# Performance work log

Measured on AMD Instinct MI355X. Metric: run time of the kernel, lower is better.

## Reference

```python
import jax, jax.numpy as jnp
import numpy as np

B, C, H, W = 2, 320, 48, 48
HEADS, DIM_HEAD, NUM_FILTERS = 8, 64, 32
INNER = HEADS * DIM_HEAD  # 512
LN_EPS = 1e-05


def setup_inputs() -> dict:
    key = jax.random.key(0)
    ks = jax.random.split(key, 8)
    w = 0.02
    return {
        "hidden_states": jax.random.normal(ks[0], (B, C, H, W), jnp.float32),
        "encoder_hidden_states": jax.random.normal(ks[1], (B, C, H, W), jnp.float32),
        "Wq": jax.random.normal(ks[2], (C, INNER), jnp.float32) * w,
        "Wk": jax.random.normal(ks[3], (C, INNER), jnp.float32) * w,
        "Wv": jax.random.normal(ks[4], (C, INNER), jnp.float32) * w,
        "Wo": jax.random.normal(ks[5], (INNER, C), jnp.float32) * w,
        "bo": jnp.zeros((C,), jnp.float32),
        "ln_gamma": jnp.ones((C,), jnp.float32),
        "ln_beta": jnp.zeros((C,), jnp.float32),
        "ex_filters": jax.random.normal(ks[6], (NUM_FILTERS, INNER), jnp.float32),
        "dist_filters": jax.random.normal(ks[7], (NUM_FILTERS, INNER), jnp.float32),
        "scale": jnp.ones((1,), jnp.float32),  # learnable scale shadows dim_head**-0.5
    }


def _split_heads(t, heads):
    b, s, d = t.shape
    return t.reshape(b, s, heads, d // heads).transpose(0, 2, 1, 3)  # [b,h,s,dh]


def reference(hidden_states, encoder_hidden_states, Wq, Wk, Wv, Wo, bo,
              ln_gamma, ln_beta, ex_filters, dist_filters, scale):
    b, c, h, w = hidden_states.shape
    _, _, rh, rw = encoder_hidden_states.shape
    residual = hidden_states
    s = scale[0]

    hs = hidden_states.transpose(0, 2, 3, 1).reshape(b, h * w, c)        # [b, q, C]
    ehs = encoder_hidden_states.transpose(0, 2, 3, 1).reshape(b, rh * rw, c)

    # LayerNorm on encoder states
    mu = ehs.mean(-1, keepdims=True)
    var = jnp.mean((ehs - mu) ** 2, axis=-1, keepdims=True)
    ehs = (ehs - mu) * jax.lax.rsqrt(var + LN_EPS) * ln_gamma + ln_beta

    q = _split_heads(hs @ Wq, HEADS)    # [b,h,q,dh]
    k = _split_heads(ehs @ Wk, HEADS)   # [b,h,kv,dh]
    v = _split_heads(ehs @ Wv, HEADS)   # [b,h,kv,dh]
    ef = _split_heads(jnp.broadcast_to(ex_filters[None], (b,) + ex_filters.shape), HEADS)   # [b,h,F,dh]
    df = _split_heads(jnp.broadcast_to(dist_filters[None], (b,) + dist_filters.shape), HEADS)

    # spatial attention: softmax over kv positions
    spatial = jax.nn.softmax(jnp.einsum('bhfd,bhkd->bhfk', ef, k) * s, axis=-1)   # [b,h,F,kv]
    # channel attention: softmax over the filter axis (torch dim=1 of [B*h, F, q])
    channel = jax.nn.softmax(jnp.einsum('bhfd,bhqd->bhfq', df, q) * s, axis=2)    # [b,h,F,q]

    attn = jnp.einsum('bhfq,bhfk->bhqk', channel, spatial)                        # [b,h,q,kv]
    out = jnp.einsum('bhqk,bhkd->bhqd', attn, v)                                  # [b,h,q,dh]

    out = out.transpose(0, 2, 1, 3).reshape(b, h * w, INNER)
    out = out @ Wo + bo
    out = out.reshape(b, h, w, c).transpose(0, 3, 1, 2)
    return out + residual * s
```

## Files before the change

### kernel.cpp

```cpp
#include <hip/hip_runtime.h>
#include <math.h>

#define Bc 2
#define Cc 320
#define Pc 2304
#define HEADSc 8
#define DHc 64
#define INNERc 512
#define Fc 32
#define LN_EPS 1e-5f
#define CHUNKS 18
#define CHUNK_P (Pc / CHUNKS)

typedef __attribute__((ext_vector_type(8))) short bf16x8;
typedef __attribute__((ext_vector_type(4))) float f32x4;

static __device__ __forceinline__ ushort f2bf(float x) {
  uint u = __builtin_bit_cast(uint, x);
  u = (u + 0x7fffu + ((u >> 16) & 1u)) >> 16;
  return (ushort)u;
}
static __device__ __forceinline__ float bf2f(ushort u) {
  return __builtin_bit_cast(float, ((uint)u) << 16);
}

__global__ __launch_bounds__(256) void stats_kernel(
    const float* __restrict__ ehs, float* __restrict__ mu,
    float* __restrict__ rstd) {
  int lane = threadIdx.x & 63, g = threadIdx.x >> 6;
  int gp = blockIdx.x * 64 + lane;
  int b = gp / Pc, p = gp % Pc;
  const float* base = ehs + (size_t)b * Cc * Pc + p;
  float sum = 0.f, sumsq = 0.f;
  for (int c = g * 80; c < (g + 1) * 80; ++c) {
    float x = base[(size_t)c * Pc];
    sum += x; sumsq += x * x;
  }
  __shared__ float s1[4][64], s2[4][64];
  s1[g][lane] = sum; s2[g][lane] = sumsq;
  __syncthreads();
  if (threadIdx.x < 64) {
    int l = threadIdx.x;
    float ts = s1[0][l] + s1[1][l] + s1[2][l] + s1[3][l];
    float tq = s2[0][l] + s2[1][l] + s2[2][l] + s2[3][l];
    float mean = ts / (float)Cc;
    float var = tq / (float)Cc - mean * mean;
    int gp2 = blockIdx.x * 64 + l;
    mu[gp2] = mean;
    rstd[gp2] = rsqrtf(var + LN_EPS);
  }
}

static __device__ void transpose_tile(const float* __restrict__ src,
                                      ushort* __restrict__ dst, int R, int C,
                                      int r0, int c0, int tid,
                                      float (*t)[65]) {
#pragma unroll
  for (int it = 0; it < 4; ++it) {
    int lin = it * 256 + tid;
    int rr = lin >> 4, c4 = lin & 15;
    float4 v = *(const float4*)(&src[(size_t)(r0 + rr) * C + c0 + c4 * 4]);
    t[rr][c4 * 4 + 0] = v.x; t[rr][c4 * 4 + 1] = v.y;
    t[rr][c4 * 4 + 2] = v.z; t[rr][c4 * 4 + 3] = v.w;
  }
  __syncthreads();
#pragma unroll
  for (int it = 0; it < 2; ++it) {
    int lin = it * 256 + tid;
    int cc = lin >> 3, r8 = lin & 7;
    ushort tmp[8];
#pragma unroll
    for (int j = 0; j < 8; ++j) tmp[j] = f2bf(t[r8 * 8 + j][cc]);
    *(uint4*)(&dst[(size_t)(c0 + cc) * R + r0 + r8 * 8]) = *(const uint4*)tmp;
  }
}

__global__ __launch_bounds__(256) void transpose_act_kernel(
    const float* __restrict__ hs, const float* __restrict__ ehs,
    const float* __restrict__ mu, const float* __restrict__ rstd,
    const float* __restrict__ gamma, const float* __restrict__ beta,
    ushort* __restrict__ hsT, ushort* __restrict__ ehsT) {
  __shared__ float t[64][65];
  __shared__ float lmu[64], lrs[64], lgam[64], lbet[64];
  int z = blockIdx.z, b = z & 1, which = z >> 1;
  int r0 = blockIdx.y * 64, c0 = blockIdx.x * 64;
  int tid = threadIdx.x;
  const float* src = (which ? ehs : hs) + (size_t)b * Cc * Pc;
  ushort* dst = (which ? ehsT : hsT) + (size_t)b * Pc * Cc;
  if (which && tid < 64) {
    lmu[tid] = mu[b * Pc + c0 + tid];
    lrs[tid] = rstd[b * Pc + c0 + tid];
    lgam[tid] = gamma[r0 + tid];
    lbet[tid] = beta[r0 + tid];
  }
#pragma unroll
  for (int it = 0; it < 4; ++it) {
    int lin = it * 256 + tid;
    int rr = lin >> 4, c4 = lin & 15;
    float4 v = *(const float4*)(&src[(size_t)(r0 + rr) * Pc + c0 + c4 * 4]);
    t[rr][c4 * 4 + 0] = v.x; t[rr][c4 * 4 + 1] = v.y;
    t[rr][c4 * 4 + 2] = v.z; t[rr][c4 * 4 + 3] = v.w;
  }
  __syncthreads();
#pragma unroll
  for (int it = 0; it < 2; ++it) {
    int lin = it * 256 + tid;
    int cc = lin >> 3, r8 = lin & 7;
    ushort tmp[8];
    float m_ = which ? lmu[cc] : 0.f, rs_ = which ? lrs[cc] : 1.f;
#pragma unroll
    for (int j = 0; j < 8; ++j) {
      int ch = r8 * 8 + j;
      float x = t[ch][cc];
      float val = which ? (x - m_) * rs_ * lgam[ch] + lbet[ch] : x;
      tmp[j] = f2bf(val);
    }
    *(uint4*)(&dst[(size_t)(c0 + cc) * Cc + r0 + r8 * 8]) = *(const uint4*)tmp;
  }
}

__global__ __launch_bounds__(256) void prep_w_kernel(
    const float* __restrict__ Wv, const float* __restrict__ Wo,
    const float* __restrict__ exf, const float* __restrict__ Wk,
    const float* __restrict__ dif, const float* __restrict__ Wq,
    ushort* __restrict__ WvT, ushort* __restrict__ WoT,
    ushort* __restrict__ Gk, ushort* __restrict__ Gq) {
  __shared__ float smem[32 * 66 + 64 * 65];
  int idx = blockIdx.x, tid = threadIdx.x;
  if (idx < 40) {
    float (*t)[65] = (float(*)[65])smem;
    transpose_tile(Wv, WvT, Cc, INNERc, (idx / 8) * 64, (idx % 8) * 64, tid, t);
  } else if (idx < 80) {
    int i = idx - 40;
    float (*t)[65] = (float(*)[65])smem;
    transpose_tile(Wo, WoT, INNERc, Cc, (i / 5) * 64, (i % 5) * 64, tid, t);
  } else {
    int i = idx - 80;
    int c0 = (i % 5) * 64, h = (i / 5) % 8, zz = i / 40;
    const float* filt = zz ? dif : exf;
    const float* W = zz ? Wq : Wk;
    ushort* G = zz ? Gq : Gk;
    float (*ef)[66] = (float(*)[66])smem;
    float (*wk)[65] = (float(*)[65])(smem + 32 * 66);
    for (int l = tid; l < Fc * DHc; l += 256) {
      int f = l >> 6, d = l & 63;
      ef[f][d] = filt[(size_t)f * INNERc + h * 64 + d];
    }
    for (int l = tid; l < 64 * DHc; l += 256) {
      int cc = l >> 6, d = l & 63;
      wk[cc][d] = W[(size_t)(c0 + cc) * INNERc + h * 64 + d];
    }
    __syncthreads();
    int f = tid >> 3, cbase = tid & 7;
    float acc[8] = {};
#pragma unroll
    for (int d4 = 0; d4 < DHc; d4 += 4) {
      float4 a = *(const float4*)(&ef[f][d4]);
#pragma unroll
      for (int j = 0; j < 8; ++j) {
        float4 b = *(const float4*)(&wk[cbase + j * 8][d4]);
        acc[j] += a.x * b.x + a.y * b.y + a.z * b.z + a.w * b.w;
      }
    }
#pragma unroll
    for (int j = 0; j < 8; ++j)
      G[(size_t)(h * Fc + f) * Cc + c0 + cbase + j * 8] = f2bf(acc[j]);
  }
}

__global__ __launch_bounds__(256) void gemm_all_kernel(
    const ushort* __restrict__ WvT, const ushort* __restrict__ Gk,
    const ushort* __restrict__ Gq, const ushort* __restrict__ ehsT,
    const ushort* __restrict__ hsT, ushort* __restrict__ Vt,
    float* __restrict__ L1, float* __restrict__ Lc) {
  const int K = Cc;
  int b = blockIdx.z, y = blockIdx.y;
  const ushort* A;
  const ushort* Bt;
  ushort* OutB = nullptr;
  float* OutF = nullptr;
  if (y < 8) {
    int m0 = y * 64;
    A = WvT + (size_t)m0 * K; Bt = ehsT;
    OutB = Vt + ((size_t)b * INNERc + m0) * Pc;
  } else if (y < 12) {
    int m0 = (y - 8) * 64;
    A = Gk + (size_t)m0 * K; Bt = ehsT;
    OutF = L1 + ((size_t)b * 256 + m0) * Pc;
  } else {
    int m0 = (y - 12) * 64;
    A = Gq + (size_t)m0 * K; Bt = hsT;
    OutF = Lc + ((size_t)b * 256 + m0) * Pc;
  }
  int n0 = blockIdx.x * 128;
  int tid = threadIdx.x, lane = tid & 63, wv = tid >> 6;
  int l15 = lane & 15, kq = lane >> 4;
  __shared__ alignas(16) ushort As[64 * 64];
  __shared__ alignas(16) ushort Bs[128 * 64];
  const ushort* Bb = Bt + ((size_t)b * Pc + n0) * K;

  f32x4 acc[4][2] = {};
  for (int k0 = 0; k0 < K; k0 += 64) {
#pragma unroll
    for (int it = 0; it < 2; ++it) {
      int lin = it * 256 + tid;
      int row = lin >> 3, p = lin & 7;
      int lc = p ^ (row & 7);
      *(uint4*)(&As[row * 64 + p * 8]) =
          *(const uint4*)(A + (size_t)row * K + k0 + lc * 8);
    }
#pragma unroll
    for (int it = 0; it < 4; ++it) {
      int lin = it * 256 + tid;
      int row = lin >> 3, p = lin & 7;
      int lc = p ^ (row & 7);
      *(uint4*)(&Bs[row * 64 + p * 8]) =
          *(const uint4*)(Bb + (size_t)row * K + k0 + lc * 8);
    }
    __syncthreads();
#pragma unroll
    for (int s = 0; s < 2; ++s) {
      bf16x8 af[4], bfr[2];
#pragma unroll
      for (int mt = 0; mt < 4; ++mt) {
        int m = mt * 16 + l15;
        int p = (s * 4 + kq) ^ (m & 7);
        af[mt] = *(const bf16x8*)(&As[m * 64 + p * 8]);
      }
#pragma unroll
      for (int nt = 0; nt < 2; ++nt) {
        int n = wv * 32 + nt * 16 + l15;
        int p = (s * 4 + kq) ^ (n & 7);
        bfr[nt] = *(const bf16x8*)(&Bs[n * 64 + p * 8]);
      }
#pragma unroll
      for (int mt = 0; mt < 4; ++mt)
#pragma unroll
        for (int nt = 0; nt < 2; ++nt)
          acc[mt][nt] = __builtin_amdgcn_mfma_f32_16x16x32_bf16(
              af[mt], bfr[nt], acc[mt][nt], 0, 0, 0);
    }
    __syncthreads();
  }
  if (OutB) {
#pragma unroll
    for (int mt = 0; mt < 4; ++mt)
#pragma unroll
      for (int nt = 0; nt < 2; ++nt) {
        int ncol = n0 + wv * 32 + nt * 16 + l15;
#pragma unroll
        for (int r = 0; r < 4; ++r) {
          int m = mt * 16 + kq * 4 + r;
          OutB[(size_t)m * Pc + ncol] = f2bf(acc[mt][nt][r]);
        }
      }
  } else {
#pragma unroll
    for (int mt = 0; mt < 4; ++mt)
#pragma unroll
      for (int nt = 0; nt < 2; ++nt) {
        int ncol = n0 + wv * 32 + nt * 16 + l15;
#pragma unroll
        for (int r = 0; r < 4; ++r) {
          int m = mt * 16 + kq * 4 + r;
          OutF[(size_t)m * Pc + ncol] = acc[mt][nt][r];
        }
      }
  }
}

__global__ __launch_bounds__(256) void rowstat_kernel(
    const float* __restrict__ L, const float* __restrict__ scale_p,
    float* __restrict__ rowm, float* __restrict__ rowinv) {
  __shared__ float red[4];
  float s = scale_p[0];
  const float* Lr = L + (size_t)blockIdx.x * Pc;
  int tid = threadIdx.x, lane = tid & 63, wv = tid >> 6;
  float vals[9];
  float m = -1e30f;
#pragma unroll
  for (int i = 0; i < 9; ++i) {
    vals[i] = Lr[tid + 256 * i] * s;
    m = fmaxf(m, vals[i]);
  }
#pragma unroll
  for (int o = 32; o > 0; o >>= 1) m = fmaxf(m, __shfl_xor(m, o));
  if (lane == 0) red[wv] = m;
  __syncthreads();
  m = fmaxf(fmaxf(red[0], red[1]), fmaxf(red[2], red[3]));
  __syncthreads();
  float sum = 0.f;
#pragma unroll
  for (int i = 0; i < 9; ++i) sum += __expf(vals[i] - m);
#pragma unroll
  for (int o = 32; o > 0; o >>= 1) sum += __shfl_xor(sum, o);
  if (lane == 0) red[wv] = sum;
  __syncthreads();
  if (tid == 0) {
    sum = red[0] + red[1] + red[2] + red[3];
    rowm[blockIdx.x] = m;
    rowinv[blockIdx.x] = 1.f / sum;
  }
}

__global__ __launch_bounds__(256) void sv_part_kernel(
    const float* __restrict__ L1, const ushort* __restrict__ Vt,
    const float* __restrict__ rowm, const float* __restrict__ rowinv,
    const float* __restrict__ scale_p, float* __restrict__ svp) {
  int b = blockIdx.z, h = blockIdx.y, c = blockIdx.x;
  int tid = threadIdx.x;
  int tx = tid & 15, ty = tid >> 4;
  int p0base = c * CHUNK_P;
  const float* sp = L1 + ((size_t)(b * HEADSc + h)) * Fc * Pc;
  const ushort* vb = Vt + ((size_t)b * INNERc + h * DHc) * Pc;

  __shared__ float sp_s[64][34];
  __shared__ float v_s[64][68];
  __shared__ float lm[Fc], li[Fc];
  if (tid < Fc) {
    int row0 = (b * HEADSc + h) * Fc;
    lm[tid] = rowm[row0 + tid];
    li[tid] = rowinv[row0 + tid];
  }
  __syncthreads();
  float s = scale_p[0];

  float acc[2][4] = {};
  for (int t = 0; t < CHUNK_P; t += 64) {
    int p0 = p0base + t;
    for (int l = tid; l < Fc * 64; l += 256) {
      int f = l >> 6, pp = l & 63;
      float raw = sp[(size_t)f * Pc + p0 + pp];
      sp_s[pp][f] = __expf(s * raw - lm[f]) * li[f];
    }
    for (int l = tid; l < DHc * 64; l += 256) {
      int d = l >> 6, pp = l & 63;
      v_s[pp][d] = bf2f(vb[(size_t)d * Pc + p0 + pp]);
    }
    __syncthreads();
#pragma unroll
    for (int kk = 0; kk < 64; ++kk) {
      float2 a = *reinterpret_cast<const float2*>(&sp_s[kk][ty * 2]);
      float4 bv = *reinterpret_cast<const float4*>(&v_s[kk][tx * 4]);
      acc[0][0] += a.x * bv.x; acc[0][1] += a.x * bv.y;
      acc[0][2] += a.x * bv.z; acc[0][3] += a.x * bv.w;
      acc[1][0] += a.y * bv.x; acc[1][1] += a.y * bv.y;
      acc[1][2] += a.y * bv.z; acc[1][3] += a.y * bv.w;
    }
    __syncthreads();
  }
  int bh = b * HEADSc + h;
  float* op = svp + ((size_t)c * 16 + bh) * (Fc * DHc);
#pragma unroll
  for (int i = 0; i < 2; ++i) {
    int f = ty * 2 + i;
    *reinterpret_cast<float4*>(&op[(size_t)f * DHc + tx * 4]) =
        make_float4(acc[i][0], acc[i][1], acc[i][2], acc[i][3]);
  }
}

__global__ __launch_bounds__(256) void sv_reduce_kernel(
    const float* __restrict__ svp, float* __restrict__ sv) {
  int idx = blockIdx.x * 256 + threadIdx.x;
  float s = 0.f;
#pragma unroll
  for (int c = 0; c < CHUNKS; ++c) s += svp[(size_t)c * 32768 + idx];
  sv[idx] = s;
}

__global__ __launch_bounds__(256) void oa_kernel(
    const float* __restrict__ Lc, const float* __restrict__ sv,
    const float* __restrict__ scale_p, ushort* __restrict__ OAT) {
  int b = blockIdx.z, h = blockIdx.y;
  int tid = threadIdx.x;
  int lane = tid & 63, wv = tid >> 6;
  int pos0 = blockIdx.x * 64;
  float s = scale_p[0];
  __shared__ float svl[Fc][DHc];
  __shared__ float tile[64][65];
  for (int l = tid; l < Fc * DHc; l += 256)
    svl[l >> 6][l & 63] = sv[((size_t)(b * HEADSc + h)) * Fc * DHc + l];
  __syncthreads();
  const float* ch = Lc + (((size_t)(b * HEADSc + h)) * Fc) * Pc + pos0 + lane;
  float v[Fc];
  float m = -1e30f;
#pragma unroll
  for (int f = 0; f < Fc; ++f) {
    v[f] = ch[(size_t)f * Pc] * s;
    m = fmaxf(m, v[f]);
  }
  float sum = 0.f;
#pragma unroll
  for (int f = 0; f < Fc; ++f) {
    v[f] = __expf(v[f] - m);
    sum += v[f];
  }
  float inv = 1.f / sum;
  float acc[16] = {};
#pragma unroll
  for (int f = 0; f < Fc; ++f) {
    float cf = v[f] * inv;
#pragma unroll
    for (int dd = 0; dd < 16; ++dd) acc[dd] += cf * svl[f][wv * 16 + dd];
  }
#pragma unroll
  for (int dd = 0; dd < 16; ++dd) tile[lane][wv * 16 + dd] = acc[dd];
  __syncthreads();
#pragma unroll
  for (int it = 0; it < 2; ++it) {
    int lin = it * 256 + tid;
    int p = lin >> 3, c8 = lin & 7;
    ushort tmp[8];
#pragma unroll
    for (int j = 0; j < 8; ++j) tmp[j] = f2bf(tile[p][c8 * 8 + j]);
    *(uint4*)(&OAT[((size_t)b * Pc + pos0 + p) * INNERc + h * DHc + c8 * 8]) =
        *(const uint4*)tmp;
  }
}

__global__ __launch_bounds__(256) void gemm_mfma_kernel(
    const ushort* __restrict__ A, const ushort* __restrict__ Bt,
    float* __restrict__ Out, int K, int Mdim,
    const float* __restrict__ bias, const float* __restrict__ res,
    const float* __restrict__ scale_p) {
  int b = blockIdx.z;
  int n0 = blockIdx.x * 128, m0 = blockIdx.y * 64;
  int tid = threadIdx.x, lane = tid & 63, wv = tid >> 6;
  int l15 = lane & 15, kq = lane >> 4;
  __shared__ alignas(16) ushort As[64 * 64];
  __shared__ alignas(16) ushort Bs[128 * 64];
  const ushort* Ab = A + (size_t)m0 * K;
  const ushort* Bb = Bt + ((size_t)b * Pc + n0) * K;

  f32x4 acc[4][2] = {};
  for (int k0 = 0; k0 < K; k0 += 64) {
#pragma unroll
    for (int it = 0; it < 2; ++it) {
      int lin = it * 256 + tid;
      int row = lin >> 3, p = lin & 7;
      int lc = p ^ (row & 7);
      *(uint4*)(&As[row * 64 + p * 8]) =
          *(const uint4*)(Ab + (size_t)row * K + k0 + lc * 8);
    }
#pragma unroll
    for (int it = 0; it < 4; ++it) {
      int lin = it * 256 + tid;
      int row = lin >> 3, p = lin & 7;
      int lc = p ^ (row & 7);
      *(uint4*)(&Bs[row * 64 + p * 8]) =
          *(const uint4*)(Bb + (size_t)row * K + k0 + lc * 8);
    }
    __syncthreads();
#pragma unroll
    for (int s = 0; s < 2; ++s) {
      bf16x8 af[4], bfr[2];
#pragma unroll
      for (int mt = 0; mt < 4; ++mt) {
        int m = mt * 16 + l15;
        int p = (s * 4 + kq) ^ (m & 7);
        af[mt] = *(const bf16x8*)(&As[m * 64 + p * 8]);
      }
#pragma unroll
      for (int nt = 0; nt < 2; ++nt) {
        int n = wv * 32 + nt * 16 + l15;
        int p = (s * 4 + kq) ^ (n & 7);
        bfr[nt] = *(const bf16x8*)(&Bs[n * 64 + p * 8]);
      }
#pragma unroll
      for (int mt = 0; mt < 4; ++mt)
#pragma unroll
        for (int nt = 0; nt < 2; ++nt)
          acc[mt][nt] = __builtin_amdgcn_mfma_f32_16x16x32_bf16(
              af[mt], bfr[nt], acc[mt][nt], 0, 0, 0);
    }
    __syncthreads();
  }
  float s = scale_p[0];
  float* Ob = Out + ((size_t)b * Mdim + m0) * Pc + n0;
  const float* rb = res + ((size_t)b * Mdim + m0) * Pc + n0;
#pragma unroll
  for (int mt = 0; mt < 4; ++mt)
#pragma unroll
    for (int nt = 0; nt < 2; ++nt) {
      int ncol = wv * 32 + nt * 16 + l15;
#pragma unroll
      for (int r = 0; r < 4; ++r) {
        int m = mt * 16 + kq * 4 + r;
        Ob[(size_t)m * Pc + ncol] =
            acc[mt][nt][r] + bias[m0 + m] + s * rb[(size_t)m * Pc + ncol];
      }
    }
}

extern "C" void kernel_launch(void* const* d_in, const int* in_sizes, int n_in,
                              void* d_out, int out_size, void* d_ws, size_t ws_size,
                              hipStream_t stream) {
  const float* hs    = (const float*)d_in[0];
  const float* ehs   = (const float*)d_in[1];
  const float* Wq    = (const float*)d_in[2];
  const float* Wk    = (const float*)d_in[3];
  const float* Wv    = (const float*)d_in[4];
  const float* Wo    = (const float*)d_in[5];
  const float* bo    = (const float*)d_in[6];
  const float* gamma = (const float*)d_in[7];
  const float* beta  = (const float*)d_in[8];
  const float* exf   = (const float*)d_in[9];
  const float* dif   = (const float*)d_in[10];
  const float* scale = (const float*)d_in[11];
  float* out = (float*)d_out;

  float* ws = (float*)d_ws;
  float* L1   = ws;
  float* Lc   = L1 + 1179648;
  float* sv   = Lc + 1179648;
  float* svp  = sv + 32768;
  float* mu   = svp + 589824;
  float* rstd = mu + 4608;
  float* rowm = rstd + 4608;
  float* rowinv = rowm + 512;
  ushort* hsT  = (ushort*)(rowinv + 512);
  ushort* ehsT = hsT + 1474560;
  ushort* WvT  = ehsT + 1474560;
  ushort* WoT  = WvT + 163840;
  ushort* Gk   = WoT + 163840;
  ushort* Gq   = Gk + 81920;
  ushort* Vt   = Gq + 81920;
  ushort* OAT  = Vt + 2359296;

  stats_kernel<<<dim3((Bc * Pc) / 64), dim3(256), 0, stream>>>(ehs, mu, rstd);
  transpose_act_kernel<<<dim3(Pc / 64, Cc / 64, 4), dim3(256), 0, stream>>>(
      hs, ehs, mu, rstd, gamma, beta, hsT, ehsT);
  prep_w_kernel<<<dim3(160), dim3(256), 0, stream>>>(
      Wv, Wo, exf, Wk, dif, Wq, WvT, WoT, Gk, Gq);
  gemm_all_kernel<<<dim3(Pc / 128, 16, Bc), dim3(256), 0, stream>>>(
      WvT, Gk, Gq, ehsT, hsT, Vt, L1, Lc);
  rowstat_kernel<<<dim3(Bc * HEADSc * Fc), dim3(256), 0, stream>>>(
      L1, scale, rowm, rowinv);
  sv_part_kernel<<<dim3(CHUNKS, HEADSc, Bc), dim3(256), 0, stream>>>(
      L1, Vt, rowm, rowinv, scale, svp);
  sv_reduce_kernel<<<dim3((16 * Fc * DHc) / 256), dim3(256), 0, stream>>>(svp, sv);
  oa_kernel<<<dim3(Pc / 64, HEADSc, Bc), dim3(256), 0, stream>>>(
      Lc, sv, scale, OAT);
  gemm_mfma_kernel<<<dim3(Pc / 128, Cc / 64, Bc), dim3(256), 0, stream>>>(
      WoT, OAT, out, INNERc, Cc, bo, hs, scale);
}
```

Before: 157.3 us.

## Fuse spatial and channel softmax into GEMM kernels with online-softmax chunk merge

Splits the combined GEMM so only V is materialized. The spatial logits are computed per 128-position chunk and fed straight into a local softmax and an MFMA-based P·V product, with per-chunk max and sum merged in the reduce step. Channel logits, their softmax over filters and the multiply with the spatial-value matrix are fused into one kernel, also on MFMA. This removes the fp32 L1/Lc round trips through global memory and the separate row-statistics and scalar-FMA kernels. In exchange the probabilities are held in bf16 and the fused kernels use more shared memory and synchronisation.

```diff
diff --git a/kernel.cpp b/kernel.cpp
--- a/kernel.cpp
+++ b/kernel.cpp
@@ -10,7 +10,7 @@
 #define Fc 32
 #define LN_EPS 1e-5f
 #define CHUNKS 18
-#define CHUNK_P (Pc / CHUNKS)
+#define CHUNK_P 128
 
 typedef __attribute__((ext_vector_type(8))) short bf16x8;
 typedef __attribute__((ext_vector_type(4))) float f32x4;
@@ -19,9 +19,6 @@
   uint u = __builtin_bit_cast(uint, x);
   u = (u + 0x7fffu + ((u >> 16) & 1u)) >> 16;
   return (ushort)u;
-}
-static __device__ __forceinline__ float bf2f(ushort u) {
-  return __builtin_bit_cast(float, ((uint)u) << 16);
 }
 
 __global__ __launch_bounds__(256) void stats_kernel(
@@ -168,36 +165,17 @@
   }
 }
 
-__global__ __launch_bounds__(256) void gemm_all_kernel(
-    const ushort* __restrict__ WvT, const ushort* __restrict__ Gk,
-    const ushort* __restrict__ Gq, const ushort* __restrict__ ehsT,
-    const ushort* __restrict__ hsT, ushort* __restrict__ Vt,
-    float* __restrict__ L1, float* __restrict__ Lc) {
+__global__ __launch_bounds__(256) void gemm_v_kernel(
+    const ushort* __restrict__ WvT, const ushort* __restrict__ ehsT,
+    ushort* __restrict__ Vt) {
   const int K = Cc;
-  int b = blockIdx.z, y = blockIdx.y;
-  const ushort* A;
-  const ushort* Bt;
-  ushort* OutB = nullptr;
-  float* OutF = nullptr;
-  if (y < 8) {
-    int m0 = y * 64;
-    A = WvT + (size_t)m0 * K; Bt = ehsT;
-    OutB = Vt + ((size_t)b * INNERc + m0) * Pc;
-  } else if (y < 12) {
-    int m0 = (y - 8) * 64;
-    A = Gk + (size_t)m0 * K; Bt = ehsT;
-    OutF = L1 + ((size_t)b * 256 + m0) * Pc;
-  } else {
-    int m0 = (y - 12) * 64;
-    A = Gq + (size_t)m0 * K; Bt = hsT;
-    OutF = Lc + ((size_t)b * 256 + m0) * Pc;
-  }
-  int n0 = blockIdx.x * 128;
+  int b = blockIdx.z, m0 = blockIdx.y * 64, n0 = blockIdx.x * 128;
   int tid = threadIdx.x, lane = tid & 63, wv = tid >> 6;
   int l15 = lane & 15, kq = lane >> 4;
   __shared__ alignas(16) ushort As[64 * 64];
   __shared__ alignas(16) ushort Bs[128 * 64];
-  const ushort* Bb = Bt + ((size_t)b * Pc + n0) * K;
+  const ushort* Ab = WvT + (size_t)m0 * K;
+  const ushort* Bb = ehsT + ((size_t)b * Pc + n0) * K;
 
   f32x4 acc[4][2] = {};
   for (int k0 = 0; k0 < K; k0 += 64) {
@@ -207,7 +185,7 @@
       int row = lin >> 3, p = lin & 7;
       int lc = p ^ (row & 7);
       *(uint4*)(&As[row * 64 + p * 8]) =
-          *(const uint4*)(A + (size_t)row * K + k0 + lc * 8);
+          *(const uint4*)(Ab + (size_t)row * K + k0 + lc * 8);
     }
 #pragma unroll
     for (int it = 0; it < 4; ++it) {
@@ -219,18 +197,18 @@
     }
     __syncthreads();
 #pragma unroll
-    for (int s = 0; s < 2; ++s) {
+    for (int ss = 0; ss < 2; ++ss) {
       bf16x8 af[4], bfr[2];
 #pragma unroll
       for (int mt = 0; mt < 4; ++mt) {
         int m = mt * 16 + l15;
-        int p = (s * 4 + kq) ^ (m & 7);
+        int p = (ss * 4 + kq) ^ (m & 7);
         af[mt] = *(const bf16x8*)(&As[m * 64 + p * 8]);
       }
 #pragma unroll
       for (int nt = 0; nt < 2; ++nt) {
         int n = wv * 32 + nt * 16 + l15;
-        int p = (s * 4 + kq) ^ (n & 7);
+        int p = (ss * 4 + kq) ^ (n & 7);
         bfr[nt] = *(const bf16x8*)(&Bs[n * 64 + p * 8]);
       }
 #pragma unroll
@@ -242,179 +220,300 @@
     }
     __syncthreads();
   }
-  if (OutB) {
-#pragma unroll
-    for (int mt = 0; mt < 4; ++mt)
+  ushort* Ob = Vt + ((size_t)b * INNERc + m0) * Pc + n0;
+#pragma unroll
+  for (int mt = 0; mt < 4; ++mt)
+#pragma unroll
+    for (int nt = 0; nt < 2; ++nt) {
+      int ncol = wv * 32 + nt * 16 + l15;
+#pragma unroll
+      for (int r = 0; r < 4; ++r) {
+        int m = mt * 16 + kq * 4 + r;
+        Ob[(size_t)m * Pc + ncol] = f2bf(acc[mt][nt][r]);
+      }
+    }
+}
+
+__global__ __launch_bounds__(256) void spatial_kernel(
+    const ushort* __restrict__ Gk, const ushort* __restrict__ ehsT,
+    const ushort* __restrict__ Vt, const float* __restrict__ scale_p,
+    float* __restrict__ svp, float* __restrict__ mj, float* __restrict__ lj) {
+  int c = blockIdx.x, h = blockIdx.y, b = blockIdx.z;
+  int tid = threadIdx.x, lane = tid & 63, wv = tid >> 6;
+  int l15 = lane & 15, kq = lane >> 4;
+  int pos0 = c * CHUNK_P;
+  int bh = b * HEADSc + h;
+  float s = scale_p[0];
+
+  __shared__ alignas(16) ushort As[32 * 64];
+  __shared__ alignas(16) ushort Bs[128 * 64];
+  __shared__ float Sq[32 * 132];
+  __shared__ alignas(16) ushort P[32 * 136];
+  __shared__ alignas(16) ushort Vs[64 * 136];
+
+  const ushort* Ab = Gk + (size_t)(h * Fc) * Cc;
+  const ushort* Bb = ehsT + ((size_t)b * Pc + pos0) * Cc;
+  f32x4 acc[2][2] = {};
+  for (int k0 = 0; k0 < Cc; k0 += 64) {
+    {
+      int row = tid >> 3, p = tid & 7;
+      int lc = p ^ (row & 7);
+      *(uint4*)(&As[row * 64 + p * 8]) =
+          *(const uint4*)(Ab + (size_t)row * Cc + k0 + lc * 8);
+    }
+#pragma unroll
+    for (int it = 0; it < 4; ++it) {
+      int lin = it * 256 + tid;
+      int row = lin >> 3, p = lin & 7;
+      int lc = p ^ (row & 7);
+      *(uint4*)(&Bs[row * 64 + p * 8]) =
+          *(const uint4*)(Bb + (size_t)row * Cc + k0 + lc * 8);
+    }
+    __syncthreads();
+#pragma unroll
+    for (int ss = 0; ss < 2; ++ss) {
+      bf16x8 af[2], bfr[2];
+#pragma unroll
+      for (int mt = 0; mt < 2; ++mt) {
+        int m = mt * 16 + l15;
+        int p = (ss * 4 + kq) ^ (m & 7);
+        af[mt] = *(const bf16x8*)(&As[m * 64 + p * 8]);
+      }
 #pragma unroll
       for (int nt = 0; nt < 2; ++nt) {
-        int ncol = n0 + wv * 32 + nt * 16 + l15;
-#pragma unroll
-        for (int r = 0; r < 4; ++r) {
-          int m = mt * 16 + kq * 4 + r;
-          OutB[(size_t)m * Pc + ncol] = f2bf(acc[mt][nt][r]);
+        int n = wv * 32 + nt * 16 + l15;
+        int p = (ss * 4 + kq) ^ (n & 7);
+        bfr[nt] = *(const bf16x8*)(&Bs[n * 64 + p * 8]);
+      }
+#pragma unroll
+      for (int mt = 0; mt < 2; ++mt)
+#pragma unroll
+        for (int nt = 0; nt < 2; ++nt)
+          acc[mt][nt] = __builtin_amdgcn_mfma_f32_16x16x32_bf16(
+              af[mt], bfr[nt], acc[mt][nt], 0, 0, 0);
+    }
+    __syncthreads();
+  }
+#pragma unroll
+  for (int mt = 0; mt < 2; ++mt)
+#pragma unroll
+    for (int nt = 0; nt < 2; ++nt)
+#pragma unroll
+      for (int r = 0; r < 4; ++r)
+        Sq[(mt * 16 + kq * 4 + r) * 132 + wv * 32 + nt * 16 + l15] =
+            acc[mt][nt][r];
+
+  {
+    const ushort* vb = Vt + ((size_t)b * INNERc + h * DHc) * Pc + pos0;
+#pragma unroll
+    for (int it = 0; it < 4; ++it) {
+      int lin = it * 256 + tid;
+      int row = lin >> 4, p = lin & 15;
+      *(uint4*)(&Vs[row * 136 + p * 8]) =
+          *(const uint4*)(vb + (size_t)row * Pc + p * 8);
+    }
+  }
+  __syncthreads();
+
+  {
+    int row = tid >> 3, sub = tid & 7;
+    float vals[16];
+    float m_ = -1e30f;
+#pragma unroll
+    for (int i = 0; i < 16; ++i) {
+      vals[i] = s * Sq[row * 132 + sub * 16 + i];
+      m_ = fmaxf(m_, vals[i]);
+    }
+    m_ = fmaxf(m_, __shfl_xor(m_, 1));
+    m_ = fmaxf(m_, __shfl_xor(m_, 2));
+    m_ = fmaxf(m_, __shfl_xor(m_, 4));
+    float l_ = 0.f;
+#pragma unroll
+    for (int i = 0; i < 16; i += 2) {
+      float e0 = __expf(vals[i] - m_);
+      float e1 = __expf(vals[i + 1] - m_);
+      l_ += e0 + e1;
+      uint pk = (uint)f2bf(e0) | ((uint)f2bf(e1) << 16);
+      *(uint*)(&P[row * 136 + sub * 16 + i]) = pk;
+    }
+    l_ += __shfl_xor(l_, 1);
+    l_ += __shfl_xor(l_, 2);
+    l_ += __shfl_xor(l_, 4);
+    if (sub == 0) {
+      mj[((size_t)c * 16 + bh) * Fc + row] = m_;
+      lj[((size_t)c * 16 + bh) * Fc + row] = l_;
+    }
+  }
+  __syncthreads();
+
+  f32x4 acc2[2] = {};
+#pragma unroll
+  for (int ss = 0; ss < 4; ++ss) {
+    bf16x8 af[2];
+#pragma unroll
+    for (int mt = 0; mt < 2; ++mt)
+      af[mt] = *(const bf16x8*)(&P[(mt * 16 + l15) * 136 + ss * 32 + kq * 8]);
+    bf16x8 bfr = *(const bf16x8*)(&Vs[(wv * 16 + l15) * 136 + ss * 32 + kq * 8]);
+#pragma unroll
+    for (int mt = 0; mt < 2; ++mt)
+      acc2[mt] = __builtin_amdgcn_mfma_f32_16x16x32_bf16(af[mt], bfr, acc2[mt],
+                                                         0, 0, 0);
+  }
+  float* op = svp + ((size_t)c * 16 + bh) * (Fc * DHc);
+#pragma unroll
+  for (int mt = 0; mt < 2; ++mt)
+#pragma unroll
+    for (int r = 0; r < 4; ++r)
+      op[(mt * 16 + kq * 4 + r) * DHc + wv * 16 + l15] = acc2[mt][r];
+}
+
+__global__ __launch_bounds__(256) void sv_reduce_kernel(
+    const float* __restrict__ svp, const float* __restrict__ mj,
+    const float* __restrict__ lj, ushort* __restrict__ svT) {
+  int idx = blockIdx.x * 256 + threadIdx.x;
+  int d = idx & 63, fr = idx >> 6;
+  int bh = fr >> 5, f = fr & 31;
+  float m = -1e30f;
+#pragma unroll
+  for (int c = 0; c < CHUNKS; ++c)
+    m = fmaxf(m, mj[((size_t)c * 16 + bh) * Fc + f]);
+  float osum = 0.f, lsum = 0.f;
+#pragma unroll
+  for (int c = 0; c < CHUNKS; ++c) {
+    float w = __expf(mj[((size_t)c * 16 + bh) * Fc + f] - m);
+    osum += w * svp[((size_t)c * 16 + bh) * (Fc * DHc) + f * DHc + d];
+    lsum += w * lj[((size_t)c * 16 + bh) * Fc + f];
+  }
+  svT[((size_t)bh * DHc + d) * Fc + f] = f2bf(osum / lsum);
+}
+
+__global__ __launch_bounds__(256) void channel_kernel(
+    const ushort* __restrict__ Gq, const ushort* __restrict__ hsT,
+    const ushort* __restrict__ svT, const float* __restrict__ scale_p,
+    ushort* __restrict__ OAT) {
+  int pb = blockIdx.x, hp = blockIdx.y, b = blockIdx.z;
+  int pos0 = pb * 64;
+  int tid = threadIdx.x, lane = tid & 63, wv = tid >> 6;
+  int l15 = lane & 15, kq = lane >> 4;
+  float s = scale_p[0];
+
+  __shared__ alignas(16) ushort Aq[2][32 * 64];
+  __shared__ alignas(16) ushort Bs[64 * 64];
+  __shared__ float SO[64 * 68];
+  __shared__ alignas(16) ushort Pt[64 * 40];
+  __shared__ alignas(16) ushort svs[64 * 40];
+  __shared__ float red[4 * 64];
+
+  f32x4 acc[2][2] = {};
+  const ushort* Bb = hsT + ((size_t)b * Pc + pos0) * Cc;
+  for (int k0 = 0; k0 < Cc; k0 += 64) {
+#pragma unroll
+    for (int it = 0; it < 2; ++it) {
+      int lin = it * 256 + tid;
+      int hh = lin >> 8, row = (lin >> 3) & 31, p = lin & 7;
+      int lc = p ^ (row & 7);
+      *(uint4*)(&Aq[hh][row * 64 + p * 8]) = *(const uint4*)(
+          Gq + (size_t)((hp * 2 + hh) * Fc + row) * Cc + k0 + lc * 8);
+    }
+#pragma unroll
+    for (int it = 0; it < 2; ++it) {
+      int lin = it * 256 + tid;
+      int row = lin >> 3, p = lin & 7;
+      int lc = p ^ (row & 7);
+      *(uint4*)(&Bs[row * 64 + p * 8]) =
+          *(const uint4*)(Bb + (size_t)row * Cc + k0 + lc * 8);
+    }
+    __syncthreads();
+#pragma unroll
+    for (int ss = 0; ss < 2; ++ss) {
+      int n = wv * 16 + l15;
+      int pb_ = (ss * 4 + kq) ^ (n & 7);
+      bf16x8 bfr = *(const bf16x8*)(&Bs[n * 64 + pb_ * 8]);
+#pragma unroll
+      for (int hh = 0; hh < 2; ++hh)
+#pragma unroll
+        for (int mt = 0; mt < 2; ++mt) {
+          int m = mt * 16 + l15;
+          int pa = (ss * 4 + kq) ^ (m & 7);
+          bf16x8 af = *(const bf16x8*)(&Aq[hh][m * 64 + pa * 8]);
+          acc[hh][mt] = __builtin_amdgcn_mfma_f32_16x16x32_bf16(
+              af, bfr, acc[hh][mt], 0, 0, 0);
         }
-      }
-  } else {
-#pragma unroll
-    for (int mt = 0; mt < 4; ++mt)
-#pragma unroll
-      for (int nt = 0; nt < 2; ++nt) {
-        int ncol = n0 + wv * 32 + nt * 16 + l15;
-#pragma unroll
-        for (int r = 0; r < 4; ++r) {
-          int m = mt * 16 + kq * 4 + r;
-          OutF[(size_t)m * Pc + ncol] = acc[mt][nt][r];
-        }
-      }
-  }
-}
-
-__global__ __launch_bounds__(256) void rowstat_kernel(
-    const float* __restrict__ L, const float* __restrict__ scale_p,
-    float* __restrict__ rowm, float* __restrict__ rowinv) {
-  __shared__ float red[4];
-  float s = scale_p[0];
-  const float* Lr = L + (size_t)blockIdx.x * Pc;
-  int tid = threadIdx.x, lane = tid & 63, wv = tid >> 6;
-  float vals[9];
-  float m = -1e30f;
-#pragma unroll
-  for (int i = 0; i < 9; ++i) {
-    vals[i] = Lr[tid + 256 * i] * s;
-    m = fmaxf(m, vals[i]);
-  }
-#pragma unroll
-  for (int o = 32; o > 0; o >>= 1) m = fmaxf(m, __shfl_xor(m, o));
-  if (lane == 0) red[wv] = m;
-  __syncthreads();
-  m = fmaxf(fmaxf(red[0], red[1]), fmaxf(red[2], red[3]));
-  __syncthreads();
-  float sum = 0.f;
-#pragma unroll
-  for (int i = 0; i < 9; ++i) sum += __expf(vals[i] - m);
-#pragma unroll
-  for (int o = 32; o > 0; o >>= 1) sum += __shfl_xor(sum, o);
-  if (lane == 0) red[wv] = sum;
-  __syncthreads();
-  if (tid == 0) {
-    sum = red[0] + red[1] + red[2] + red[3];
-    rowm[blockIdx.x] = m;
-    rowinv[blockIdx.x] = 1.f / sum;
-  }
-}
-
-__global__ __launch_bounds__(256) void sv_part_kernel(
-    const float* __restrict__ L1, const ushort* __restrict__ Vt,
-    const float* __restrict__ rowm, const float* __restrict__ rowinv,
-    const float* __restrict__ scale_p, float* __restrict__ svp) {
-  int b = blockIdx.z, h = blockIdx.y, c = blockIdx.x;
-  int tid = threadIdx.x;
-  int tx = tid & 15, ty = tid >> 4;
-  int p0base = c * CHUNK_P;
-  const float* sp = L1 + ((size_t)(b * HEADSc + h)) * Fc * Pc;
-  const ushort* vb = Vt + ((size_t)b * INNERc + h * DHc) * Pc;
-
-  __shared__ float sp_s[64][34];
-  __shared__ float v_s[64][68];
-  __shared__ float lm[Fc], li[Fc];
-  if (tid < Fc) {
-    int row0 = (b * HEADSc + h) * Fc;
-    lm[tid] = rowm[row0 + tid];
-    li[tid] = rowinv[row0 + tid];
-  }
-  __syncthreads();
-  float s = scale_p[0];
-
-  float acc[2][4] = {};
-  for (int t = 0; t < CHUNK_P; t += 64) {
-    int p0 = p0base + t;
-    for (int l = tid; l < Fc * 64; l += 256) {
-      int f = l >> 6, pp = l & 63;
-      float raw = sp[(size_t)f * Pc + p0 + pp];
-      sp_s[pp][f] = __expf(s * raw - lm[f]) * li[f];
-    }
-    for (int l = tid; l < DHc * 64; l += 256) {
-      int d = l >> 6, pp = l & 63;
-      v_s[pp][d] = bf2f(vb[(size_t)d * Pc + p0 + pp]);
-    }
-    __syncthreads();
-#pragma unroll
-    for (int kk = 0; kk < 64; ++kk) {
-      float2 a = *reinterpret_cast<const float2*>(&sp_s[kk][ty * 2]);
-      float4 bv = *reinterpret_cast<const float4*>(&v_s[kk][tx * 4]);
-      acc[0][0] += a.x * bv.x; acc[0][1] += a.x * bv.y;
-      acc[0][2] += a.x * bv.z; acc[0][3] += a.x * bv.w;
-      acc[1][0] += a.y * bv.x; acc[1][1] += a.y * bv.y;
-      acc[1][2] += a.y * bv.z; acc[1][3] += a.y * bv.w;
-    }
-    __syncthreads();
-  }
-  int bh = b * HEADSc + h;
-  float* op = svp + ((size_t)c * 16 + bh) * (Fc * DHc);
-#pragma unroll
-  for (int i = 0; i < 2; ++i) {
-    int f = ty * 2 + i;
-    *reinterpret_cast<float4*>(&op[(size_t)f * DHc + tx * 4]) =
-        make_float4(acc[i][0], acc[i][1], acc[i][2], acc[i][3]);
-  }
-}
-
-__global__ __launch_bounds__(256) void sv_reduce_kernel(
-    const float* __restrict__ svp, float* __restrict__ sv) {
-  int idx = blockIdx.x * 256 + threadIdx.x;
-  float s = 0.f;
-#pragma unroll
-  for (int c = 0; c < CHUNKS; ++c) s += svp[(size_t)c * 32768 + idx];
-  sv[idx] = s;
-}
-
-__global__ __launch_bounds__(256) void oa_kernel(
-    const float* __restrict__ Lc, const float* __restrict__ sv,
-    const float* __restrict__ scale_p, ushort* __restrict__ OAT) {
-  int b = blockIdx.z, h = blockIdx.y;
-  int tid = threadIdx.x;
-  int lane = tid & 63, wv = tid >> 6;
-  int pos0 = blockIdx.x * 64;
-  float s = scale_p[0];
-  __shared__ float svl[Fc][DHc];
-  __shared__ float tile[64][65];
-  for (int l = tid; l < Fc * DHc; l += 256)
-    svl[l >> 6][l & 63] = sv[((size_t)(b * HEADSc + h)) * Fc * DHc + l];
-  __syncthreads();
-  const float* ch = Lc + (((size_t)(b * HEADSc + h)) * Fc) * Pc + pos0 + lane;
-  float v[Fc];
-  float m = -1e30f;
-#pragma unroll
-  for (int f = 0; f < Fc; ++f) {
-    v[f] = ch[(size_t)f * Pc] * s;
-    m = fmaxf(m, v[f]);
-  }
-  float sum = 0.f;
-#pragma unroll
-  for (int f = 0; f < Fc; ++f) {
-    v[f] = __expf(v[f] - m);
-    sum += v[f];
-  }
-  float inv = 1.f / sum;
-  float acc[16] = {};
-#pragma unroll
-  for (int f = 0; f < Fc; ++f) {
-    float cf = v[f] * inv;
-#pragma unroll
-    for (int dd = 0; dd < 16; ++dd) acc[dd] += cf * svl[f][wv * 16 + dd];
-  }
-#pragma unroll
-  for (int dd = 0; dd < 16; ++dd) tile[lane][wv * 16 + dd] = acc[dd];
-  __syncthreads();
-#pragma unroll
-  for (int it = 0; it < 2; ++it) {
-    int lin = it * 256 + tid;
-    int p = lin >> 3, c8 = lin & 7;
-    ushort tmp[8];
-#pragma unroll
-    for (int j = 0; j < 8; ++j) tmp[j] = f2bf(tile[p][c8 * 8 + j]);
-    *(uint4*)(&OAT[((size_t)b * Pc + pos0 + p) * INNERc + h * DHc + c8 * 8]) =
-        *(const uint4*)tmp;
+    }
+    __syncthreads();
+  }
+
+  for (int hh = 0; hh < 2; ++hh) {
+    int h = hp * 2 + hh;
+#pragma unroll
+    for (int mt = 0; mt < 2; ++mt)
+#pragma unroll
+      for (int r = 0; r < 4; ++r)
+        SO[(mt * 16 + kq * 4 + r) * 68 + wv * 16 + l15] = acc[hh][mt][r];
+    {
+      int rr = tid >> 2, p = tid & 3;
+      *(uint4*)(&svs[rr * 40 + p * 8]) = *(const uint4*)(
+          svT + ((size_t)(b * HEADSc + h) * DHc + rr) * Fc + p * 8);
+    }
+    __syncthreads();
+    {
+      int pos = tid & 63, g = tid >> 6;
+      float v8[8];
+      float pm = -1e30f;
+#pragma unroll
+      for (int i = 0; i < 8; ++i) {
+        v8[i] = s * SO[(g * 8 + i) * 68 + pos];
+        pm = fmaxf(pm, v8[i]);
+      }
+      red[g * 64 + pos] = pm;
+      __syncthreads();
+      float m_ = fmaxf(fmaxf(red[pos], red[64 + pos]),
+                       fmaxf(red[128 + pos], red[192 + pos]));
+      __syncthreads();
+      float ps = 0.f;
+#pragma unroll
+      for (int i = 0; i < 8; ++i) {
+        v8[i] = __expf(v8[i] - m_);
+        ps += v8[i];
+      }
+      red[g * 64 + pos] = ps;
+      __syncthreads();
+      float inv = 1.f / (red[pos] + red[64 + pos] + red[128 + pos] +
+                         red[192 + pos]);
+#pragma unroll
+      for (int i = 0; i < 8; i += 2) {
+        uint pk = (uint)f2bf(v8[i] * inv) | ((uint)f2bf(v8[i + 1] * inv) << 16);
+        *(uint*)(&Pt[pos * 40 + g * 8 + i]) = pk;
+      }
+    }
+    __syncthreads();
+    {
+      bf16x8 b_ = *(const bf16x8*)(&svs[(wv * 16 + l15) * 40 + kq * 8]);
+      f32x4 acc3[4];
+#pragma unroll
+      for (int mt = 0; mt < 4; ++mt) {
+        bf16x8 a_ = *(const bf16x8*)(&Pt[(mt * 16 + l15) * 40 + kq * 8]);
+        f32x4 z = {0.f, 0.f, 0.f, 0.f};
+        acc3[mt] = __builtin_amdgcn_mfma_f32_16x16x32_bf16(a_, b_, z, 0, 0, 0);
+      }
+#pragma unroll
+      for (int mt = 0; mt < 4; ++mt)
+#pragma unroll
+        for (int r = 0; r < 4; ++r)
+          SO[(mt * 16 + kq * 4 + r) * 68 + wv * 16 + l15] = acc3[mt][r];
+    }
+    __syncthreads();
+#pragma unroll
+    for (int it = 0; it < 2; ++it) {
+      int lin = it * 256 + tid;
+      int p = lin >> 3, c8 = lin & 7;
+      ushort tmp[8];
+#pragma unroll
+      for (int j = 0; j < 8; ++j) tmp[j] = f2bf(SO[p * 68 + c8 * 8 + j]);
+      *(uint4*)(&OAT[((size_t)b * Pc + pos0 + p) * INNERc + h * 64 + c8 * 8]) =
+          *(const uint4*)tmp;
+    }
+    __syncthreads();
   }
 }
 
@@ -452,18 +551,18 @@
     }
     __syncthreads();
 #pragma unroll
-    for (int s = 0; s < 2; ++s) {
+    for (int ss = 0; ss < 2; ++ss) {
       bf16x8 af[4], bfr[2];
 #pragma unroll
       for (int mt = 0; mt < 4; ++mt) {
         int m = mt * 16 + l15;
-        int p = (s * 4 + kq) ^ (m & 7);
+        int p = (ss * 4 + kq) ^ (m & 7);
         af[mt] = *(const bf16x8*)(&As[m * 64 + p * 8]);
       }
 #pragma unroll
       for (int nt = 0; nt < 2; ++nt) {
         int n = wv * 32 + nt * 16 + l15;
-        int p = (s * 4 + kq) ^ (n & 7);
+        int p = (ss * 4 + kq) ^ (n & 7);
         bfr[nt] = *(const bf16x8*)(&Bs[n * 64 + p * 8]);
       }
 #pragma unroll
@@ -510,21 +609,19 @@
   float* out = (float*)d_out;
 
   float* ws = (float*)d_ws;
-  float* L1   = ws;
-  float* Lc   = L1 + 1179648;
-  float* sv   = Lc + 1179648;
-  float* svp  = sv + 32768;
-  float* mu   = svp + 589824;
+  float* svp  = ws;
+  float* mj   = svp + 589824;
+  float* lj   = mj + 9216;
+  float* mu   = lj + 9216;
   float* rstd = mu + 4608;
-  float* rowm = rstd + 4608;
-  float* rowinv = rowm + 512;
-  ushort* hsT  = (ushort*)(rowinv + 512);
+  ushort* hsT  = (ushort*)(rstd + 4608);
   ushort* ehsT = hsT + 1474560;
   ushort* WvT  = ehsT + 1474560;
   ushort* WoT  = WvT + 163840;
   ushort* Gk   = WoT + 163840;
   ushort* Gq   = Gk + 81920;
-  ushort* Vt   = Gq + 81920;
+  ushort* svT  = Gq + 81920;
+  ushort* Vt   = svT + 32768;
   ushort* OAT  = Vt + 2359296;
 
   stats_kernel<<<dim3((Bc * Pc) / 64), dim3(256), 0, stream>>>(ehs, mu, rstd);
@@ -532,15 +629,13 @@
       hs, ehs, mu, rstd, gamma, beta, hsT, ehsT);
   prep_w_kernel<<<dim3(160), dim3(256), 0, stream>>>(
       Wv, Wo, exf, Wk, dif, Wq, WvT, WoT, Gk, Gq);
-  gemm_all_kernel<<<dim3(Pc / 128, 16, Bc), dim3(256), 0, stream>>>(
-      WvT, Gk, Gq, ehsT, hsT, Vt, L1, Lc);
-  rowstat_kernel<<<dim3(Bc * HEADSc * Fc), dim3(256), 0, stream>>>(
-      L1, scale, rowm, rowinv);
-  sv_part_kernel<<<dim3(CHUNKS, HEADSc, Bc), dim3(256), 0, stream>>>(
-      L1, Vt, rowm, rowinv, scale, svp);
-  sv_reduce_kernel<<<dim3((16 * Fc * DHc) / 256), dim3(256), 0, stream>>>(svp, sv);
-  oa_kernel<<<dim3(Pc / 64, HEADSc, Bc), dim3(256), 0, stream>>>(
-      Lc, sv, scale, OAT);
+  gemm_v_kernel<<<dim3(Pc / 128, INNERc / 64, Bc), dim3(256), 0, stream>>>(
+      WvT, ehsT, Vt);
+  spatial_kernel<<<dim3(CHUNKS, HEADSc, Bc), dim3(256), 0, stream>>>(
+      Gk, ehsT, Vt, scale, svp, mj, lj);
+  sv_reduce_kernel<<<dim3(128), dim3(256), 0, stream>>>(svp, mj, lj, svT);
+  channel_kernel<<<dim3(Pc / 64, HEADSc / 2, Bc), dim3(256), 0, stream>>>(
+      Gq, hsT, svT, scale, OAT);
   gemm_mfma_kernel<<<dim3(Pc / 128, Cc / 64, Bc), dim3(256), 0, stream>>>(
       WoT, OAT, out, INNERc, Cc, bo, hs, scale);
 }
```

Result: no change. 155.9 us (-0.9%).
